# Optimization experiments

Measured on AMD Instinct MI355X. Metric: run time of the kernel, lower is better.

The kernel has to match this reference:

```python
import jax, jax.numpy as jnp
import numpy as np
from jax import lax


def _binarize(t):
    # sign binarization to +1/-1 (zero maps to -1, matching torch.where(t > 0, 1, -1))
    return jnp.where(t > 0, 1.0, -1.0).astype(t.dtype)


def _bconv(x, w, b):
    # binary conv: binarize input and weights, then standard 3x3 'same' conv
    y = lax.conv_general_dilated(
        _binarize(x), _binarize(w),
        window_strides=(1, 1), padding=((1, 1), (1, 1)),
        dimension_numbers=('NCHW', 'OIHW', 'NCHW'))
    return y + b[None, :, None, None]


def _maxpool2(x):
    return lax.reduce_window(x, -jnp.inf, lax.max, (1, 1, 2, 2), (1, 1, 2, 2), 'VALID')


def setup_inputs() -> dict:
    key = jax.random.key(0)
    ks = jax.random.split(key, 13)
    s = 0.1
    return {
        'x': jax.random.normal(ks[0], (4096, 1, 28, 28), jnp.float32),
        'w1': jax.random.normal(ks[1], (32, 1, 3, 3), jnp.float32) * s,
        'b1': jax.random.normal(ks[2], (32,), jnp.float32) * s,
        'w2': jax.random.normal(ks[3], (64, 32, 3, 3), jnp.float32) * s,
        'b2': jax.random.normal(ks[4], (64,), jnp.float32) * s,
        'w3': jax.random.normal(ks[5], (16, 64, 3, 3), jnp.float32) * s,
        'b3': jax.random.normal(ks[6], (16,), jnp.float32) * s,
        'fc1_w': jax.random.normal(ks[7], (256, 16 * 7 * 7), jnp.float32) * s,
        'fc1_b': jax.random.normal(ks[8], (256,), jnp.float32) * s,
        'fc2_w': jax.random.normal(ks[9], (128, 256), jnp.float32) * s,
        'fc2_b': jax.random.normal(ks[10], (128,), jnp.float32) * s,
        'fc3_w': jax.random.normal(ks[11], (10, 128), jnp.float32) * s,
        'fc3_b': jax.random.normal(ks[12], (10,), jnp.float32) * s,
    }


def reference(x, w1, b1, w2, b2, w3, b3, fc1_w, fc1_b, fc2_w, fc2_b, fc3_w, fc3_b):
    h = jax.nn.relu(_maxpool2(_bconv(x, w1, b1)))      # [B,32,14,14]
    h = jax.nn.relu(_maxpool2(_bconv(h, w2, b2)))      # [B,64,7,7]
    h = jax.nn.relu(_bconv(h, w3, b3))                 # [B,16,7,7]
    h = h.reshape(-1, 16 * 7 * 7)
    h = jax.nn.relu(h @ fc1_w.T + fc1_b)
    h = jax.nn.relu(h @ fc2_w.T + fc2_b)
    return h @ fc3_w.T + fc3_b                          # [B,10]
```

## Files before the change

### kernel.cpp

```cpp
#include <hip/hip_runtime.h>
#include <cstdint>

#define OFF_PW    0
#define OFF_W1T   4096
#define OFF_W2T   823296
#define OFF_H3T   954368
#define OFF_H1T   14061568
#define OFF_H2T   18255872

__global__ __launch_bounds__(256) void prep(
    const float* __restrict__ w1, const float* __restrict__ w2,
    const float* __restrict__ w3,
    const float* __restrict__ fc1_w, const float* __restrict__ fc2_w,
    uint32_t* __restrict__ pw, float* __restrict__ w1T, float* __restrict__ w2T) {
    int t = threadIdx.x;
    if (blockIdx.x == 0) {
        if (t < 32) {
            uint32_t b = 0;
            for (int k = 0; k < 9; ++k) b |= (w1[t * 9 + k] > 0.f ? 1u : 0u) << k;
            pw[t] = b;
        }
        for (int idx = t; idx < 576; idx += 256) {
            int oc = idx / 9, tap = idx % 9;
            int kh = tap / 3, kw = tap % 3;
            uint32_t b = 0;
            for (int ic = 0; ic < 32; ++ic)
                b |= (w2[((oc * 32 + ic) * 3 + kh) * 3 + kw] > 0.f ? 1u : 0u) << ic;
            pw[32 + idx] = b;
        }
        for (int idx = t; idx < 144; idx += 256) {
            int oc = idx / 9, tap = idx % 9;
            int kh = tap / 3, kw = tap % 3;
            uint32_t lo = 0, hi = 0;
            for (int ic = 0; ic < 32; ++ic) {
                lo |= (w3[((oc * 64 + ic) * 3 + kh) * 3 + kw] > 0.f ? 1u : 0u) << ic;
                hi |= (w3[((oc * 64 + ic + 32) * 3 + kh) * 3 + kw] > 0.f ? 1u : 0u) << ic;
            }
            pw[608 + idx * 2] = lo;
            pw[608 + idx * 2 + 1] = hi;
        }
    } else {
        int e = (blockIdx.x - 1) * 256 + t;
        if (e < 204800) {
            int k = e >> 8, n = e & 255;
            w1T[e] = (k < 784) ? fc1_w[n * 784 + k] : 0.f;
        } else {
            int e2 = e - 204800;
            int k = e2 >> 7, n = e2 & 127;
            w2T[e2] = fc2_w[n * 256 + k];
        }
    }
}

__global__ __launch_bounds__(256) void conv_stack(
    const float* __restrict__ x,
    const float* __restrict__ b1, const float* __restrict__ b2,
    const float* __restrict__ b3,
    const uint32_t* __restrict__ pw,
    float* __restrict__ h3T) {
    __shared__ uint32_t s_wb1[32];
    __shared__ uint32_t s_W2[576];
    __shared__ uint32_t s_W3[288];
    __shared__ float s_b1[32], s_b2[64], s_b3[16];
    __shared__ uint32_t s_xrow[28];
    __shared__ uint32_t s_H1[256];
    __shared__ uint32_t s_H2[162];

    const int t = threadIdx.x;
    const int img = blockIdx.x;

    s_H1[t] = 0;
    if (t < 162) s_H2[t] = 0;
    if (t < 32) { s_wb1[t] = pw[t]; s_b1[t] = b1[t]; }
    if (t >= 32 && t < 96) s_b2[t - 32] = b2[t - 32];
    if (t >= 96 && t < 112) s_b3[t - 96] = b3[t - 96];
    for (int i = t; i < 576; i += 256) s_W2[i] = pw[32 + i];
    for (int i = t; i < 288; i += 256) s_W3[i] = pw[608 + i];
    if (t >= 192 && t < 220) {
        int r = t - 192;
        const float* xr = x + img * 784 + r * 28;
        uint32_t b = 0;
        for (int j = 0; j < 28; ++j) b |= (xr[j] > 0.f ? 1u : 0u) << j;
        s_xrow[r] = b;
    }
    __syncthreads();

    if (t < 196) {
        int pi = t / 14, pj = t % 14;
        uint32_t sarr[4], marr[4];
        int pcm[4];
#pragma unroll
        for (int p = 0; p < 4; ++p) {
            int i = 2 * pi + (p >> 1), j = 2 * pj + (p & 1);
            uint32_t sb = 0, mb = 0;
            int bit = 0;
#pragma unroll
            for (int di = -1; di <= 1; ++di) {
                int y = i + di;
                bool rv = (unsigned)y < 28u;
                uint32_t row = rv ? s_xrow[rv ? y : 0] : 0u;
#pragma unroll
                for (int dj = -1; dj <= 1; ++dj) {
                    int xx = j + dj;
                    bool v = rv && (unsigned)xx < 28u;
                    if (v) {
                        mb |= 1u << bit;
                        sb |= ((row >> xx) & 1u) << bit;
                    }
                    ++bit;
                }
            }
            sarr[p] = sb; marr[p] = mb; pcm[p] = __popc(mb);
        }
        uint32_t word = 0;
#pragma unroll
        for (int c = 0; c < 32; ++c) {
            uint32_t w = s_wb1[c];
            int best = -1000;
#pragma unroll
            for (int p = 0; p < 4; ++p) {
                int v = pcm[p] - 2 * __popc((sarr[p] ^ w) & marr[p]);
                best = v > best ? v : best;
            }
            word |= ((float)best + s_b1[c] > 0.f ? 1u : 0u) << c;
        }
        s_H1[(pi + 1) * 16 + (pj + 1)] = word;
    }
    __syncthreads();

    for (int task = t; task < 400; task += 256) {
        int q = task / 25, ip = task - q * 25;
        int pi = ip / 5 + 1, pj = ip % 5 + 1;
        uint32_t cell[16];
#pragma unroll
        for (int r = 0; r < 4; ++r)
#pragma unroll
            for (int c = 0; c < 4; ++c)
                cell[r * 4 + c] = s_H1[(2 * pi + r) * 16 + (2 * pj + c)];
        uint32_t nib = 0;
#pragma unroll
        for (int o = 0; o < 4; ++o) {
            int oc = q * 4 + o;
            const uint32_t* wrow = &s_W2[oc * 9];
            int best = -100000;
#pragma unroll
            for (int a = 0; a < 2; ++a)
#pragma unroll
                for (int b = 0; b < 2; ++b) {
                    int S = 0;
#pragma unroll
                    for (int kh = 0; kh < 3; ++kh)
#pragma unroll
                        for (int kw = 0; kw < 3; ++kw)
                            S += __popc(cell[(a + kh) * 4 + (b + kw)] ^ wrow[kh * 3 + kw]);
                    int v = 288 - 2 * S;
                    best = v > best ? v : best;
                }
            nib |= ((float)best + s_b2[oc] > 0.f ? 1u : 0u) << (oc & 31);
        }
        atomicOr((unsigned int*)&s_H2[((pi + 1) * 9 + (pj + 1)) * 2 + (q >> 3)],
                 (unsigned int)nib);
    }
    for (int task = t; task < 384; task += 256) {
        int q = task / 24, bp = task - q * 24;
        int pi, pj;
        if (bp < 7)       { pi = 0; pj = bp; }
        else if (bp < 14) { pi = 6; pj = bp - 7; }
        else if (bp < 19) { pi = bp - 13; pj = 0; }
        else              { pi = bp - 18; pj = 6; }
        uint32_t vr[4], vc[4];
#pragma unroll
        for (int r = 0; r < 4; ++r) {
            vr[r] = ((unsigned)(2 * pi - 1 + r) < 14u) ? 0xFFFFFFFFu : 0u;
            vc[r] = ((unsigned)(2 * pj - 1 + r) < 14u) ? 0xFFFFFFFFu : 0u;
        }
        uint32_t cell[16], V[16];
#pragma unroll
        for (int r = 0; r < 4; ++r)
#pragma unroll
            for (int c = 0; c < 4; ++c) {
                cell[r * 4 + c] = s_H1[(2 * pi + r) * 16 + (2 * pj + c)];
                V[r * 4 + c] = vr[r] & vc[c];
            }
        int nvp[4];
#pragma unroll
        for (int a = 0; a < 2; ++a)
#pragma unroll
            for (int b = 0; b < 2; ++b) {
                int i = 2 * pi + a, j = 2 * pj + b;
                int vy = 3 - (i == 0) - (i == 13);
                int vx = 3 - (j == 0) - (j == 13);
                nvp[a * 2 + b] = 32 * vy * vx;
            }
        uint32_t nib = 0;
#pragma unroll
        for (int o = 0; o < 4; ++o) {
            int oc = q * 4 + o;
            const uint32_t* wrow = &s_W2[oc * 9];
            int best = -100000;
#pragma unroll
            for (int a = 0; a < 2; ++a)
#pragma unroll
                for (int b = 0; b < 2; ++b) {
                    int S = 0;
#pragma unroll
                    for (int kh = 0; kh < 3; ++kh)
#pragma unroll
                        for (int kw = 0; kw < 3; ++kw) {
                            int ci = (a + kh) * 4 + (b + kw);
                            S += __popc((cell[ci] ^ wrow[kh * 3 + kw]) & V[ci]);
                        }
                    int v = nvp[a * 2 + b] - 2 * S;
                    best = v > best ? v : best;
                }
            nib |= ((float)best + s_b2[oc] > 0.f ? 1u : 0u) << (oc & 31);
        }
        atomicOr((unsigned int*)&s_H2[((pi + 1) * 9 + (pj + 1)) * 2 + (q >> 3)],
                 (unsigned int)nib);
    }
    __syncthreads();

    for (int task = t; task < 784; task += 256) {
        int oc = task / 49, pos = task - oc * 49;
        int pi = pos / 7, pj = pos % 7;
        uint32_t vr[3], vc[3];
#pragma unroll
        for (int d = 0; d < 3; ++d) {
            vr[d] = ((unsigned)(pi - 1 + d) < 7u) ? 0xFFFFFFFFu : 0u;
            vc[d] = ((unsigned)(pj - 1 + d) < 7u) ? 0xFFFFFFFFu : 0u;
        }
        int vy = 3 - (pi == 0) - (pi == 6);
        int vx = 3 - (pj == 0) - (pj == 6);
        int Nv = 64 * vy * vx;
        const uint32_t* wr = &s_W3[oc * 18];
        int S = 0;
#pragma unroll
        for (int kh = 0; kh < 3; ++kh)
#pragma unroll
            for (int kw = 0; kw < 3; ++kw) {
                uint32_t V = vr[kh] & vc[kw];
                int idx = ((pi + kh) * 9 + (pj + kw)) * 2;
                S += __popc((s_H2[idx] ^ wr[(kh * 3 + kw) * 2]) & V);
                S += __popc((s_H2[idx + 1] ^ wr[(kh * 3 + kw) * 2 + 1]) & V);
            }
        float h = (float)(Nv - 2 * S) + s_b3[oc];
        h3T[task * 4096 + img] = h > 0.f ? h : 0.f;
    }
}

__global__ __launch_bounds__(256) void fc1_gemm(
    const float* __restrict__ aT,
    const float* __restrict__ bT,
    const float* __restrict__ bias,
    float* __restrict__ oT) {
    const int KC = 80, LD = 68;
    __shared__ float As[KC * LD];
    __shared__ float Bs[KC * LD];
    const int t = threadIdx.x;
    const int tx = t & 15, ty = t >> 4;
    const int img0 = blockIdx.x * 64;
    const int n0 = blockIdx.y * 64;
    float acc[4][4] = {{0.f}};

    for (int kc = 0; kc < 800; kc += KC) {
#pragma unroll
        for (int s = 0; s < 5; ++s) {
            int v = t + s * 256;
            int kk = v >> 4, i4 = (v & 15) * 4;
            *(float4*)&As[kk * LD + i4] =
                *(const float4*)&aT[(kc + kk) * 4096 + img0 + i4];
            *(float4*)&Bs[kk * LD + i4] =
                *(const float4*)&bT[(kc + kk) * 256 + n0 + i4];
        }
        __syncthreads();
#pragma unroll 4
        for (int kk = 0; kk < KC; ++kk) {
            float4 a = *(const float4*)&As[kk * LD + ty * 4];
            float4 b = *(const float4*)&Bs[kk * LD + tx * 4];
            acc[0][0] += a.x * b.x; acc[0][1] += a.x * b.y;
            acc[0][2] += a.x * b.z; acc[0][3] += a.x * b.w;
            acc[1][0] += a.y * b.x; acc[1][1] += a.y * b.y;
            acc[1][2] += a.y * b.z; acc[1][3] += a.y * b.w;
            acc[2][0] += a.z * b.x; acc[2][1] += a.z * b.y;
            acc[2][2] += a.z * b.z; acc[2][3] += a.z * b.w;
            acc[3][0] += a.w * b.x; acc[3][1] += a.w * b.y;
            acc[3][2] += a.w * b.z; acc[3][3] += a.w * b.w;
        }
        __syncthreads();
    }
    float4 bb = *(const float4*)&bias[n0 + tx * 4];
    float bv[4] = {bb.x, bb.y, bb.z, bb.w};
#pragma unroll
    for (int jj = 0; jj < 4; ++jj) {
        float4 ov;
        ov.x = acc[0][jj] + bv[jj]; ov.x = ov.x > 0.f ? ov.x : 0.f;
        ov.y = acc[1][jj] + bv[jj]; ov.y = ov.y > 0.f ? ov.y : 0.f;
        ov.z = acc[2][jj] + bv[jj]; ov.z = ov.z > 0.f ? ov.z : 0.f;
        ov.w = acc[3][jj] + bv[jj]; ov.w = ov.w > 0.f ? ov.w : 0.f;
        *(float4*)&oT[(n0 + tx * 4 + jj) * 4096 + img0 + ty * 4] = ov;
    }
}

__global__ __launch_bounds__(256) void fc2_gemm(
    const float* __restrict__ aT,
    const float* __restrict__ bT,
    const float* __restrict__ bias,
    float* __restrict__ oT) {
    const int KC = 64, LDA = 68, LDB = 36;
    __shared__ float As[KC * LDA];
    __shared__ float Bs[KC * LDB];
    const int t = threadIdx.x;
    const int tx = t & 15, ty = t >> 4;
    const int img0 = blockIdx.x * 64;
    const int n0 = blockIdx.y * 32;
    float acc[4][2] = {{0.f}};

    for (int kc = 0; kc < 256; kc += KC) {
#pragma unroll
        for (int s = 0; s < 4; ++s) {
            int v = t + s * 256;
            int kk = v >> 4, i4 = (v & 15) * 4;
            *(float4*)&As[kk * LDA + i4] =
                *(const float4*)&aT[(kc + kk) * 4096 + img0 + i4];
        }
#pragma unroll
        for (int s = 0; s < 2; ++s) {
            int v = t + s * 256;
            int kk = v >> 3, n4 = (v & 7) * 4;
            *(float4*)&Bs[kk * LDB + n4] =
                *(const float4*)&bT[(kc + kk) * 128 + n0 + n4];
        }
        __syncthreads();
#pragma unroll 4
        for (int kk = 0; kk < KC; ++kk) {
            float4 a = *(const float4*)&As[kk * LDA + ty * 4];
            float2 b = *(const float2*)&Bs[kk * LDB + tx * 2];
            acc[0][0] += a.x * b.x; acc[0][1] += a.x * b.y;
            acc[1][0] += a.y * b.x; acc[1][1] += a.y * b.y;
            acc[2][0] += a.z * b.x; acc[2][1] += a.z * b.y;
            acc[3][0] += a.w * b.x; acc[3][1] += a.w * b.y;
        }
        __syncthreads();
    }
#pragma unroll
    for (int j = 0; j < 2; ++j) {
        int n = n0 + tx * 2 + j;
        float bj = bias[n];
        float4 ov;
        ov.x = acc[0][j] + bj; ov.x = ov.x > 0.f ? ov.x : 0.f;
        ov.y = acc[1][j] + bj; ov.y = ov.y > 0.f ? ov.y : 0.f;
        ov.z = acc[2][j] + bj; ov.z = ov.z > 0.f ? ov.z : 0.f;
        ov.w = acc[3][j] + bj; ov.w = ov.w > 0.f ? ov.w : 0.f;
        *(float4*)&oT[n * 4096 + img0 + ty * 4] = ov;
    }
}

__global__ __launch_bounds__(256) void fc3_gemm(
    const float* __restrict__ aT,
    const float* __restrict__ w,
    const float* __restrict__ bias,
    float* __restrict__ out) {
    int id = blockIdx.x * 256 + threadIdx.x;
    int n = id >> 12, img = id & 4095;
    const float* wr = w + n * 128;
    float a0 = 0.f, a1 = 0.f, a2 = 0.f, a3 = 0.f;
#pragma unroll 8
    for (int k = 0; k < 128; k += 4) {
        a0 += aT[(k + 0) * 4096 + img] * wr[k + 0];
        a1 += aT[(k + 1) * 4096 + img] * wr[k + 1];
        a2 += aT[(k + 2) * 4096 + img] * wr[k + 2];
        a3 += aT[(k + 3) * 4096 + img] * wr[k + 3];
    }
    out[img * 10 + n] = (a0 + a1) + (a2 + a3) + bias[n];
}

extern "C" void kernel_launch(void* const* d_in, const int* in_sizes, int n_in,
                              void* d_out, int out_size, void* d_ws, size_t ws_size,
                              hipStream_t stream) {
    const float* x     = (const float*)d_in[0];
    const float* w1    = (const float*)d_in[1];
    const float* b1    = (const float*)d_in[2];
    const float* w2    = (const float*)d_in[3];
    const float* b2    = (const float*)d_in[4];
    const float* w3    = (const float*)d_in[5];
    const float* b3    = (const float*)d_in[6];
    const float* fc1_w = (const float*)d_in[7];
    const float* fc1_b = (const float*)d_in[8];
    const float* fc2_w = (const float*)d_in[9];
    const float* fc2_b = (const float*)d_in[10];
    const float* fc3_w = (const float*)d_in[11];
    const float* fc3_b = (const float*)d_in[12];
    float* out = (float*)d_out;

    const int B = in_sizes[0] / 784;
    char* ws = (char*)d_ws;
    uint32_t* pw = (uint32_t*)(ws + OFF_PW);
    float* w1T = (float*)(ws + OFF_W1T);
    float* w2T = (float*)(ws + OFF_W2T);
    float* h3T = (float*)(ws + OFF_H3T);
    float* h1T = (float*)(ws + OFF_H1T);
    float* h2T = (float*)(ws + OFF_H2T);

    hipLaunchKernelGGL(prep, dim3(929), dim3(256), 0, stream,
                       w1, w2, w3, fc1_w, fc2_w, pw, w1T, w2T);
    hipLaunchKernelGGL(conv_stack, dim3(B), dim3(256), 0, stream,
                       x, b1, b2, b3, pw, h3T);
    hipLaunchKernelGGL(fc1_gemm, dim3(B / 64, 4), dim3(256), 0, stream,
                       h3T, w1T, fc1_b, h1T);
    hipLaunchKernelGGL(fc2_gemm, dim3(B / 64, 4), dim3(256), 0, stream,
                       h1T, w2T, fc2_b, h2T);
    hipLaunchKernelGGL(fc3_gemm, dim3(B * 10 / 256), dim3(256), 0, stream,
                       h2T, fc3_w, fc3_b, out);
}
```

Baseline: 220.1 us.

## Batch eight images per conv block and retile FC GEMMs

The conv stack now processes eight images per block. conv2 and conv3 are remapped so that each lane owns an output channel and results are packed with wave ballots. Interior positions use a popcount-threshold test with the bias folded into an integer threshold, and border positions get a separate correction path. The prep kernel is flattened into one linear index space and now also zero-pads the h3T tail. fc1 and fc2 are retiled with larger K chunks and smaller N and M tiles, which adds blocks at the cost of more shared memory per block.

```diff
diff --git a/kernel.cpp b/kernel.cpp
--- a/kernel.cpp
+++ b/kernel.cpp
@@ -12,327 +12,330 @@
     const float* __restrict__ w1, const float* __restrict__ w2,
     const float* __restrict__ w3,
     const float* __restrict__ fc1_w, const float* __restrict__ fc2_w,
-    uint32_t* __restrict__ pw, float* __restrict__ w1T, float* __restrict__ w2T) {
-    int t = threadIdx.x;
-    if (blockIdx.x == 0) {
-        if (t < 32) {
-            uint32_t b = 0;
-            for (int k = 0; k < 9; ++k) b |= (w1[t * 9 + k] > 0.f ? 1u : 0u) << k;
-            pw[t] = b;
-        }
-        for (int idx = t; idx < 576; idx += 256) {
-            int oc = idx / 9, tap = idx % 9;
-            int kh = tap / 3, kw = tap % 3;
-            uint32_t b = 0;
-            for (int ic = 0; ic < 32; ++ic)
-                b |= (w2[((oc * 32 + ic) * 3 + kh) * 3 + kw] > 0.f ? 1u : 0u) << ic;
-            pw[32 + idx] = b;
-        }
-        for (int idx = t; idx < 144; idx += 256) {
-            int oc = idx / 9, tap = idx % 9;
-            int kh = tap / 3, kw = tap % 3;
-            uint32_t lo = 0, hi = 0;
-            for (int ic = 0; ic < 32; ++ic) {
-                lo |= (w3[((oc * 64 + ic) * 3 + kh) * 3 + kw] > 0.f ? 1u : 0u) << ic;
-                hi |= (w3[((oc * 64 + ic + 32) * 3 + kh) * 3 + kw] > 0.f ? 1u : 0u) << ic;
-            }
-            pw[608 + idx * 2] = lo;
-            pw[608 + idx * 2 + 1] = hi;
-        }
+    uint32_t* __restrict__ pw, float* __restrict__ w1T,
+    float* __restrict__ w2T, float* __restrict__ h3T) {
+    int idx = blockIdx.x * 256 + threadIdx.x;
+    if (idx < 204800) {
+        int k = idx >> 8, n = idx & 255;
+        w1T[idx] = (k < 784) ? fc1_w[n * 784 + k] : 0.f;
+        return;
+    }
+    idx -= 204800;
+    if (idx < 32768) {
+        int k = idx >> 7, n = idx & 127;
+        w2T[idx] = fc2_w[n * 256 + k];
+        return;
+    }
+    idx -= 32768;
+    if (idx < 65536) {
+        h3T[784 * 4096 + idx] = 0.f;
+        return;
+    }
+    idx -= 65536;
+    if (idx >= 896) return;
+    if (idx < 32) {
+        uint32_t b = 0;
+#pragma unroll
+        for (int k = 0; k < 9; ++k) b |= (w1[idx * 9 + k] > 0.f ? 1u : 0u) << k;
+        pw[idx] = b;
+    } else if (idx < 608) {
+        int e = idx - 32;
+        int oc = e / 9, tap = e - oc * 9;
+        uint32_t b = 0;
+#pragma unroll
+        for (int ic = 0; ic < 32; ++ic)
+            b |= (w2[(oc * 32 + ic) * 9 + tap] > 0.f ? 1u : 0u) << ic;
+        pw[idx] = b;
     } else {
-        int e = (blockIdx.x - 1) * 256 + t;
-        if (e < 204800) {
-            int k = e >> 8, n = e & 255;
-            w1T[e] = (k < 784) ? fc1_w[n * 784 + k] : 0.f;
+        int e = idx - 608;
+        int oc = e / 18, r = e - oc * 18;
+        int tap = r >> 1, half = r & 1;
+        uint32_t b = 0;
+#pragma unroll
+        for (int ic = 0; ic < 32; ++ic)
+            b |= (w3[(oc * 64 + half * 32 + ic) * 9 + tap] > 0.f ? 1u : 0u) << ic;
+        pw[idx] = b;
+    }
+}
+
+__device__ __forceinline__ uint32_t bfe3(uint32_t r, int j) { return (r >> j) & 7u; }
+
+__global__ __launch_bounds__(256, 2) void conv_stack(
+    const float* __restrict__ x, const float* __restrict__ b1,
+    const float* __restrict__ b2, const float* __restrict__ b3,
+    const uint32_t* __restrict__ pw, float* __restrict__ h3T) {
+    __shared__ uint32_t s_xr[8 * 36];
+    __shared__ uint32_t s_H1[8 * 260];
+    __shared__ uint32_t s_H2[8 * 164];
+    __shared__ uint32_t s_w1[32];
+    __shared__ int s_sth1[32], s_ic1[32], s_ic2[64];
+    __shared__ uint32_t s_W2t[576];
+    __shared__ uint32_t s_W3t[288];
+    __shared__ float s_b3[16];
+
+    const int t = threadIdx.x;
+    const int lane = t & 63;
+    const int wid = t >> 6;
+    const int img0 = blockIdx.x * 8;
+
+    for (int i = t; i < 8 * 260; i += 256) s_H1[i] = 0;
+    for (int i = t; i < 8 * 164; i += 256) s_H2[i] = 0;
+    if (t < 224) {
+        int im = t / 28, row = t - im * 28;
+        const float4* xr = (const float4*)(x + (img0 + im) * 784 + row * 28);
+        uint32_t b = 0;
+#pragma unroll
+        for (int q = 0; q < 7; ++q) {
+            float4 v = xr[q];
+            b |= (v.x > 0.f ? 1u : 0u) << (q * 4 + 0);
+            b |= (v.y > 0.f ? 1u : 0u) << (q * 4 + 1);
+            b |= (v.z > 0.f ? 1u : 0u) << (q * 4 + 2);
+            b |= (v.w > 0.f ? 1u : 0u) << (q * 4 + 3);
+        }
+        s_xr[im * 36 + row] = b << 1;
+    }
+    if (t < 32) {
+        s_w1[t] = pw[t];
+        int ic = (int)floorf(-b1[t]) + 1;
+        s_ic1[t] = ic;
+        s_sth1[t] = (9 - ic) >> 1;
+    } else if (t >= 32 && t < 96) {
+        s_ic2[t - 32] = (int)floorf(-b2[t - 32]) + 1;
+    } else if (t >= 96 && t < 112) {
+        s_b3[t - 96] = b3[t - 96];
+    }
+    for (int i = t; i < 576; i += 256)
+        s_W2t[i] = pw[32 + (i & 63) * 9 + (i >> 6)];
+    for (int i = t; i < 288; i += 256)
+        s_W3t[i] = pw[608 + (i & 15) * 18 + (i >> 4)];
+    __syncthreads();
+
+    for (int task = t; task < 1568; task += 256) {
+        int pid = task >> 3, im = task & 7;
+        int pi, pj;
+        if (pid < 144) { pi = 1 + pid / 12; pj = 1 + pid - (pid / 12) * 12; }
+        else {
+            int b = pid - 144;
+            if (b < 14)      { pi = 0;  pj = b; }
+            else if (b < 28) { pi = 13; pj = b - 14; }
+            else if (b < 40) { pi = 1 + (b - 28); pj = 0; }
+            else             { pi = 1 + (b - 40); pj = 13; }
+        }
+        const uint32_t* xr = &s_xr[im * 36];
+        int y0 = 2 * pi - 1;
+        uint32_t r0 = (pi > 0)  ? xr[y0]     : 0u;
+        uint32_t r1 = xr[y0 + 1];
+        uint32_t r2 = xr[y0 + 2];
+        uint32_t r3 = (pi < 13) ? xr[y0 + 3] : 0u;
+        int j0 = 2 * pj, j1 = 2 * pj + 1;
+        uint32_t s00 = bfe3(r0, j0) | (bfe3(r1, j0) << 3) | (bfe3(r2, j0) << 6);
+        uint32_t s01 = bfe3(r0, j1) | (bfe3(r1, j1) << 3) | (bfe3(r2, j1) << 6);
+        uint32_t s10 = bfe3(r1, j0) | (bfe3(r2, j0) << 3) | (bfe3(r3, j0) << 6);
+        uint32_t s11 = bfe3(r1, j1) | (bfe3(r2, j1) << 3) | (bfe3(r3, j1) << 6);
+        uint32_t word = 0;
+        if (pid < 144) {
+#pragma unroll
+            for (int c = 0; c < 32; ++c) {
+                uint32_t w = s_w1[c];
+                int S = min(min(__popc(s00 ^ w), __popc(s01 ^ w)),
+                            min(__popc(s10 ^ w), __popc(s11 ^ w)));
+                word |= (uint32_t)(S <= s_sth1[c]) << c;
+            }
         } else {
-            int e2 = e - 204800;
-            int k = e2 >> 7, n = e2 & 127;
-            w2T[e2] = fc2_w[n * 256 + k];
-        }
-    }
-}
-
-__global__ __launch_bounds__(256) void conv_stack(
-    const float* __restrict__ x,
-    const float* __restrict__ b1, const float* __restrict__ b2,
-    const float* __restrict__ b3,
-    const uint32_t* __restrict__ pw,
-    float* __restrict__ h3T) {
-    __shared__ uint32_t s_wb1[32];
-    __shared__ uint32_t s_W2[576];
-    __shared__ uint32_t s_W3[288];
-    __shared__ float s_b1[32], s_b2[64], s_b3[16];
-    __shared__ uint32_t s_xrow[28];
-    __shared__ uint32_t s_H1[256];
-    __shared__ uint32_t s_H2[162];
-
-    const int t = threadIdx.x;
-    const int img = blockIdx.x;
-
-    s_H1[t] = 0;
-    if (t < 162) s_H2[t] = 0;
-    if (t < 32) { s_wb1[t] = pw[t]; s_b1[t] = b1[t]; }
-    if (t >= 32 && t < 96) s_b2[t - 32] = b2[t - 32];
-    if (t >= 96 && t < 112) s_b3[t - 96] = b3[t - 96];
-    for (int i = t; i < 576; i += 256) s_W2[i] = pw[32 + i];
-    for (int i = t; i < 288; i += 256) s_W3[i] = pw[608 + i];
-    if (t >= 192 && t < 220) {
-        int r = t - 192;
-        const float* xr = x + img * 784 + r * 28;
-        uint32_t b = 0;
-        for (int j = 0; j < 28; ++j) b |= (xr[j] > 0.f ? 1u : 0u) << j;
-        s_xrow[r] = b;
+            uint32_t iT = (pi == 0)  ? 0x7u   : 0u;
+            uint32_t iB = (pi == 13) ? 0x1C0u : 0u;
+            uint32_t iL = (pj == 0)  ? 0x49u  : 0u;
+            uint32_t iR = (pj == 13) ? 0x124u : 0u;
+            uint32_t i00 = iT | iL, i01 = iT | iR, i10 = iB | iL, i11 = iB | iR;
+            int n00 = 9 - __popc(i00), n01 = 9 - __popc(i01);
+            int n10 = 9 - __popc(i10), n11 = 9 - __popc(i11);
+#pragma unroll
+            for (int c = 0; c < 32; ++c) {
+                uint32_t w = s_w1[c];
+                int v0 = n00 - 2 * (__popc(s00 ^ w) - __popc(w & i00));
+                int v1 = n01 - 2 * (__popc(s01 ^ w) - __popc(w & i01));
+                int v2 = n10 - 2 * (__popc(s10 ^ w) - __popc(w & i10));
+                int v3 = n11 - 2 * (__popc(s11 ^ w) - __popc(w & i11));
+                int vm = max(max(v0, v1), max(v2, v3));
+                word |= (uint32_t)(vm >= s_ic1[c]) << c;
+            }
+        }
+        s_H1[im * 260 + (pi + 1) * 16 + (pj + 1)] = word;
     }
     __syncthreads();
 
-    if (t < 196) {
-        int pi = t / 14, pj = t % 14;
-        uint32_t sarr[4], marr[4];
-        int pcm[4];
-#pragma unroll
-        for (int p = 0; p < 4; ++p) {
-            int i = 2 * pi + (p >> 1), j = 2 * pj + (p & 1);
-            uint32_t sb = 0, mb = 0;
-            int bit = 0;
-#pragma unroll
-            for (int di = -1; di <= 1; ++di) {
-                int y = i + di;
-                bool rv = (unsigned)y < 28u;
-                uint32_t row = rv ? s_xrow[rv ? y : 0] : 0u;
-#pragma unroll
-                for (int dj = -1; dj <= 1; ++dj) {
-                    int xx = j + dj;
-                    bool v = rv && (unsigned)xx < 28u;
-                    if (v) {
-                        mb |= 1u << bit;
-                        sb |= ((row >> xx) & 1u) << bit;
-                    }
-                    ++bit;
+    {
+        uint32_t w0 = s_W2t[0 * 64 + lane], w1r = s_W2t[1 * 64 + lane],
+                 w2r = s_W2t[2 * 64 + lane], w3r = s_W2t[3 * 64 + lane],
+                 w4 = s_W2t[4 * 64 + lane], w5 = s_W2t[5 * 64 + lane],
+                 w6 = s_W2t[6 * 64 + lane], w7 = s_W2t[7 * 64 + lane],
+                 w8 = s_W2t[8 * 64 + lane];
+        int ic2 = s_ic2[lane];
+        int sth2 = (288 - ic2) >> 1;
+        int pc0 = __popc(w0), pc1 = __popc(w1r), pc2 = __popc(w2r);
+        int pc3 = __popc(w3r), pc5 = __popc(w5), pc6 = __popc(w6);
+        int pc7 = __popc(w7), pc8 = __popc(w8);
+        int topc = pc0 + pc1 + pc2, botc = pc6 + pc7 + pc8;
+        int lefc = pc0 + pc3 + pc6, rigc = pc2 + pc5 + pc8;
+
+        for (int wt = wid; wt < 392; wt += 4) {
+            int im = wt & 7, pos = wt >> 3;
+            int pi, pj;
+            if (pos < 25) { pi = 1 + pos / 5; pj = 1 + pos - (pos / 5) * 5; }
+            else {
+                int b = pos - 25;
+                if (b < 7)       { pi = 0; pj = b; }
+                else if (b < 14) { pi = 6; pj = b - 7; }
+                else if (b < 19) { pi = b - 13; pj = 0; }
+                else             { pi = b - 18; pj = 6; }
+            }
+            int base = im * 260 + 2 * pi * 16 + 2 * pj;
+            uint2 ra0 = *(const uint2*)&s_H1[base],      ra1 = *(const uint2*)&s_H1[base + 2];
+            uint2 rb0 = *(const uint2*)&s_H1[base + 16], rb1 = *(const uint2*)&s_H1[base + 18];
+            uint2 rc0 = *(const uint2*)&s_H1[base + 32], rc1 = *(const uint2*)&s_H1[base + 34];
+            uint2 rd0 = *(const uint2*)&s_H1[base + 48], rd1 = *(const uint2*)&s_H1[base + 50];
+            uint32_t c00 = ra0.x, c01 = ra0.y, c02 = ra1.x, c03 = ra1.y;
+            uint32_t c10 = rb0.x, c11 = rb0.y, c12 = rb1.x, c13 = rb1.y;
+            uint32_t c20 = rc0.x, c21 = rc0.y, c22 = rc1.x, c23 = rc1.y;
+            uint32_t c30 = rd0.x, c31 = rd0.y, c32 = rd1.x, c33 = rd1.y;
+            int S00 = __popc(c00 ^ w0) + __popc(c01 ^ w1r) + __popc(c02 ^ w2r)
+                    + __popc(c10 ^ w3r) + __popc(c11 ^ w4) + __popc(c12 ^ w5)
+                    + __popc(c20 ^ w6) + __popc(c21 ^ w7) + __popc(c22 ^ w8);
+            int S01 = __popc(c01 ^ w0) + __popc(c02 ^ w1r) + __popc(c03 ^ w2r)
+                    + __popc(c11 ^ w3r) + __popc(c12 ^ w4) + __popc(c13 ^ w5)
+                    + __popc(c21 ^ w6) + __popc(c22 ^ w7) + __popc(c23 ^ w8);
+            int S10 = __popc(c10 ^ w0) + __popc(c11 ^ w1r) + __popc(c12 ^ w2r)
+                    + __popc(c20 ^ w3r) + __popc(c21 ^ w4) + __popc(c22 ^ w5)
+                    + __popc(c30 ^ w6) + __popc(c31 ^ w7) + __popc(c32 ^ w8);
+            int S11 = __popc(c11 ^ w0) + __popc(c12 ^ w1r) + __popc(c13 ^ w2r)
+                    + __popc(c21 ^ w3r) + __popc(c22 ^ w4) + __popc(c23 ^ w5)
+                    + __popc(c31 ^ w6) + __popc(c32 ^ w7) + __popc(c33 ^ w8);
+            int pred;
+            if (pos < 25) {
+                int Sm = min(min(S00, S01), min(S10, S11));
+                pred = (Sm <= sth2);
+            } else {
+                int vmax;
+                {
+                    int rI = (pi == 0), cI = (pj == 0);
+                    int corr = (rI ? topc : 0) + (cI ? lefc : 0) - ((rI & cI) ? pc0 : 0);
+                    int nv = 32 * (9 - 3 * rI - 3 * cI + (rI & cI));
+                    vmax = nv - 2 * (S00 - corr);
                 }
-            }
-            sarr[p] = sb; marr[p] = mb; pcm[p] = __popc(mb);
-        }
-        uint32_t word = 0;
-#pragma unroll
-        for (int c = 0; c < 32; ++c) {
-            uint32_t w = s_wb1[c];
-            int best = -1000;
-#pragma unroll
-            for (int p = 0; p < 4; ++p) {
-                int v = pcm[p] - 2 * __popc((sarr[p] ^ w) & marr[p]);
-                best = v > best ? v : best;
-            }
-            word |= ((float)best + s_b1[c] > 0.f ? 1u : 0u) << c;
-        }
-        s_H1[(pi + 1) * 16 + (pj + 1)] = word;
+                {
+                    int rI = (pi == 0), cI = (pj == 6);
+                    int corr = (rI ? topc : 0) + (cI ? rigc : 0) - ((rI & cI) ? pc2 : 0);
+                    int nv = 32 * (9 - 3 * rI - 3 * cI + (rI & cI));
+                    vmax = max(vmax, nv - 2 * (S01 - corr));
+                }
+                {
+                    int rI = (pi == 6), cI = (pj == 0);
+                    int corr = (rI ? botc : 0) + (cI ? lefc : 0) - ((rI & cI) ? pc6 : 0);
+                    int nv = 32 * (9 - 3 * rI - 3 * cI + (rI & cI));
+                    vmax = max(vmax, nv - 2 * (S10 - corr));
+                }
+                {
+                    int rI = (pi == 6), cI = (pj == 6);
+                    int corr = (rI ? botc : 0) + (cI ? rigc : 0) - ((rI & cI) ? pc8 : 0);
+                    int nv = 32 * (9 - 3 * rI - 3 * cI + (rI & cI));
+                    vmax = max(vmax, nv - 2 * (S11 - corr));
+                }
+                pred = (vmax >= ic2);
+            }
+            unsigned long long m = __ballot(pred);
+            if (lane == 0) {
+                *(uint2*)&s_H2[im * 164 + ((pi + 1) * 9 + (pj + 1)) * 2] =
+                    make_uint2((uint32_t)m, (uint32_t)(m >> 32));
+            }
+        }
     }
     __syncthreads();
 
-    for (int task = t; task < 400; task += 256) {
-        int q = task / 25, ip = task - q * 25;
-        int pi = ip / 5 + 1, pj = ip % 5 + 1;
-        uint32_t cell[16];
-#pragma unroll
-        for (int r = 0; r < 4; ++r)
-#pragma unroll
-            for (int c = 0; c < 4; ++c)
-                cell[r * 4 + c] = s_H1[(2 * pi + r) * 16 + (2 * pj + c)];
-        uint32_t nib = 0;
-#pragma unroll
-        for (int o = 0; o < 4; ++o) {
-            int oc = q * 4 + o;
-            const uint32_t* wrow = &s_W2[oc * 9];
-            int best = -100000;
-#pragma unroll
-            for (int a = 0; a < 2; ++a)
-#pragma unroll
-                for (int b = 0; b < 2; ++b) {
-                    int S = 0;
-#pragma unroll
-                    for (int kh = 0; kh < 3; ++kh)
-#pragma unroll
-                        for (int kw = 0; kw < 3; ++kw)
-                            S += __popc(cell[(a + kh) * 4 + (b + kw)] ^ wrow[kh * 3 + kw]);
-                    int v = 288 - 2 * S;
-                    best = v > best ? v : best;
+    {
+        int oc = lane & 15, iq = lane >> 4;
+        uint32_t w[18];
+#pragma unroll
+        for (int k = 0; k < 18; ++k) w[k] = s_W3t[k * 16 + oc];
+        float bias3 = s_b3[oc];
+        int pc[9];
+#pragma unroll
+        for (int k = 0; k < 9; ++k) pc[k] = __popc(w[2 * k]) + __popc(w[2 * k + 1]);
+        int topc = pc[0] + pc[1] + pc[2], botc = pc[6] + pc[7] + pc[8];
+        int lefc = pc[0] + pc[3] + pc[6], rigc = pc[2] + pc[5] + pc[8];
+
+        for (int wt = wid; wt < 98; wt += 4) {
+            int iq2 = wt & 1, pos = wt >> 1;
+            int im = iq2 * 4 + iq;
+            int pi, pj;
+            if (pos < 25) { pi = 1 + pos / 5; pj = 1 + pos - (pos / 5) * 5; }
+            else {
+                int b = pos - 25;
+                if (b < 7)       { pi = 0; pj = b; }
+                else if (b < 14) { pi = 6; pj = b - 7; }
+                else if (b < 19) { pi = b - 13; pj = 0; }
+                else             { pi = b - 18; pj = 6; }
+            }
+            const uint32_t* hp = &s_H2[im * 164];
+            int S = 0;
+#pragma unroll
+            for (int kh = 0; kh < 3; ++kh)
+#pragma unroll
+                for (int kw = 0; kw < 3; ++kw) {
+                    uint2 cc = *(const uint2*)&hp[((pi + kh) * 9 + (pj + kw)) * 2];
+                    int k = kh * 3 + kw;
+                    S += __popc(cc.x ^ w[2 * k]) + __popc(cc.y ^ w[2 * k + 1]);
                 }
-            nib |= ((float)best + s_b2[oc] > 0.f ? 1u : 0u) << (oc & 31);
-        }
-        atomicOr((unsigned int*)&s_H2[((pi + 1) * 9 + (pj + 1)) * 2 + (q >> 3)],
-                 (unsigned int)nib);
-    }
-    for (int task = t; task < 384; task += 256) {
-        int q = task / 24, bp = task - q * 24;
-        int pi, pj;
-        if (bp < 7)       { pi = 0; pj = bp; }
-        else if (bp < 14) { pi = 6; pj = bp - 7; }
-        else if (bp < 19) { pi = bp - 13; pj = 0; }
-        else              { pi = bp - 18; pj = 6; }
-        uint32_t vr[4], vc[4];
-#pragma unroll
-        for (int r = 0; r < 4; ++r) {
-            vr[r] = ((unsigned)(2 * pi - 1 + r) < 14u) ? 0xFFFFFFFFu : 0u;
-            vc[r] = ((unsigned)(2 * pj - 1 + r) < 14u) ? 0xFFFFFFFFu : 0u;
-        }
-        uint32_t cell[16], V[16];
-#pragma unroll
-        for (int r = 0; r < 4; ++r)
-#pragma unroll
-            for (int c = 0; c < 4; ++c) {
-                cell[r * 4 + c] = s_H1[(2 * pi + r) * 16 + (2 * pj + c)];
-                V[r * 4 + c] = vr[r] & vc[c];
-            }
-        int nvp[4];
-#pragma unroll
-        for (int a = 0; a < 2; ++a)
-#pragma unroll
-            for (int b = 0; b < 2; ++b) {
-                int i = 2 * pi + a, j = 2 * pj + b;
-                int vy = 3 - (i == 0) - (i == 13);
-                int vx = 3 - (j == 0) - (j == 13);
-                nvp[a * 2 + b] = 32 * vy * vx;
-            }
-        uint32_t nib = 0;
-#pragma unroll
-        for (int o = 0; o < 4; ++o) {
-            int oc = q * 4 + o;
-            const uint32_t* wrow = &s_W2[oc * 9];
-            int best = -100000;
-#pragma unroll
-            for (int a = 0; a < 2; ++a)
-#pragma unroll
-                for (int b = 0; b < 2; ++b) {
-                    int S = 0;
-#pragma unroll
-                    for (int kh = 0; kh < 3; ++kh)
-#pragma unroll
-                        for (int kw = 0; kw < 3; ++kw) {
-                            int ci = (a + kh) * 4 + (b + kw);
-                            S += __popc((cell[ci] ^ wrow[kh * 3 + kw]) & V[ci]);
-                        }
-                    int v = nvp[a * 2 + b] - 2 * S;
-                    best = v > best ? v : best;
-                }
-            nib |= ((float)best + s_b2[oc] > 0.f ? 1u : 0u) << (oc & 31);
-        }
-        atomicOr((unsigned int*)&s_H2[((pi + 1) * 9 + (pj + 1)) * 2 + (q >> 3)],
-                 (unsigned int)nib);
-    }
-    __syncthreads();
-
-    for (int task = t; task < 784; task += 256) {
-        int oc = task / 49, pos = task - oc * 49;
-        int pi = pos / 7, pj = pos % 7;
-        uint32_t vr[3], vc[3];
-#pragma unroll
-        for (int d = 0; d < 3; ++d) {
-            vr[d] = ((unsigned)(pi - 1 + d) < 7u) ? 0xFFFFFFFFu : 0u;
-            vc[d] = ((unsigned)(pj - 1 + d) < 7u) ? 0xFFFFFFFFu : 0u;
-        }
-        int vy = 3 - (pi == 0) - (pi == 6);
-        int vx = 3 - (pj == 0) - (pj == 6);
-        int Nv = 64 * vy * vx;
-        const uint32_t* wr = &s_W3[oc * 18];
-        int S = 0;
-#pragma unroll
-        for (int kh = 0; kh < 3; ++kh)
-#pragma unroll
-            for (int kw = 0; kw < 3; ++kw) {
-                uint32_t V = vr[kh] & vc[kw];
-                int idx = ((pi + kh) * 9 + (pj + kw)) * 2;
-                S += __popc((s_H2[idx] ^ wr[(kh * 3 + kw) * 2]) & V);
-                S += __popc((s_H2[idx + 1] ^ wr[(kh * 3 + kw) * 2 + 1]) & V);
-            }
-        float h = (float)(Nv - 2 * S) + s_b3[oc];
-        h3T[task * 4096 + img] = h > 0.f ? h : 0.f;
-    }
-}
-
-__global__ __launch_bounds__(256) void fc1_gemm(
-    const float* __restrict__ aT,
-    const float* __restrict__ bT,
-    const float* __restrict__ bias,
-    float* __restrict__ oT) {
-    const int KC = 80, LD = 68;
-    __shared__ float As[KC * LD];
-    __shared__ float Bs[KC * LD];
-    const int t = threadIdx.x;
-    const int tx = t & 15, ty = t >> 4;
-    const int img0 = blockIdx.x * 64;
-    const int n0 = blockIdx.y * 64;
-    float acc[4][4] = {{0.f}};
-
-    for (int kc = 0; kc < 800; kc += KC) {
-#pragma unroll
-        for (int s = 0; s < 5; ++s) {
-            int v = t + s * 256;
-            int kk = v >> 4, i4 = (v & 15) * 4;
-            *(float4*)&As[kk * LD + i4] =
-                *(const float4*)&aT[(kc + kk) * 4096 + img0 + i4];
-            *(float4*)&Bs[kk * LD + i4] =
-                *(const float4*)&bT[(kc + kk) * 256 + n0 + i4];
-        }
-        __syncthreads();
-#pragma unroll 4
-        for (int kk = 0; kk < KC; ++kk) {
-            float4 a = *(const float4*)&As[kk * LD + ty * 4];
-            float4 b = *(const float4*)&Bs[kk * LD + tx * 4];
-            acc[0][0] += a.x * b.x; acc[0][1] += a.x * b.y;
-            acc[0][2] += a.x * b.z; acc[0][3] += a.x * b.w;
-            acc[1][0] += a.y * b.x; acc[1][1] += a.y * b.y;
-            acc[1][2] += a.y * b.z; acc[1][3] += a.y * b.w;
-            acc[2][0] += a.z * b.x; acc[2][1] += a.z * b.y;
-            acc[2][2] += a.z * b.z; acc[2][3] += a.z * b.w;
-            acc[3][0] += a.w * b.x; acc[3][1] += a.w * b.y;
-            acc[3][2] += a.w * b.z; acc[3][3] += a.w * b.w;
-        }
-        __syncthreads();
-    }
-    float4 bb = *(const float4*)&bias[n0 + tx * 4];
-    float bv[4] = {bb.x, bb.y, bb.z, bb.w};
-#pragma unroll
-    for (int jj = 0; jj < 4; ++jj) {
-        float4 ov;
-        ov.x = acc[0][jj] + bv[jj]; ov.x = ov.x > 0.f ? ov.x : 0.f;
-        ov.y = acc[1][jj] + bv[jj]; ov.y = ov.y > 0.f ? ov.y : 0.f;
-        ov.z = acc[2][jj] + bv[jj]; ov.z = ov.z > 0.f ? ov.z : 0.f;
-        ov.w = acc[3][jj] + bv[jj]; ov.w = ov.w > 0.f ? ov.w : 0.f;
-        *(float4*)&oT[(n0 + tx * 4 + jj) * 4096 + img0 + ty * 4] = ov;
-    }
-}
-
-__global__ __launch_bounds__(256) void fc2_gemm(
-    const float* __restrict__ aT,
-    const float* __restrict__ bT,
-    const float* __restrict__ bias,
-    float* __restrict__ oT) {
-    const int KC = 64, LDA = 68, LDB = 36;
-    __shared__ float As[KC * LDA];
-    __shared__ float Bs[KC * LDB];
+            int v;
+            if (pos < 25) {
+                v = 576 - 2 * S;
+            } else {
+                int rT = (pi == 0), rB = (pi == 6), cL = (pj == 0), cR = (pj == 6);
+                int rA = rT | rB, cA = cL | cR;
+                int corr = (rT ? topc : 0) + (rB ? botc : 0) +
+                           (cL ? lefc : 0) + (cR ? rigc : 0);
+                if (rT & cL) corr -= pc[0];
+                if (rT & cR) corr -= pc[2];
+                if (rB & cL) corr -= pc[6];
+                if (rB & cR) corr -= pc[8];
+                int nInv = 3 * rA + 3 * cA - (rA & cA);
+                v = 64 * (9 - nInv) - 2 * (S - corr);
+            }
+            float h = fmaxf((float)v + bias3, 0.f);
+            h3T[(oc * 49 + pi * 7 + pj) * 4096 + img0 + im] = h;
+        }
+    }
+}
+
+__global__ __launch_bounds__(256, 2) void fc1_gemm(
+    const float* __restrict__ aT, const float* __restrict__ bT,
+    const float* __restrict__ bias, float* __restrict__ oT) {
+    const int LDA = 68, LDB = 36;
+    __shared__ float As[160 * LDA];
+    __shared__ float Bs[160 * LDB];
     const int t = threadIdx.x;
     const int tx = t & 15, ty = t >> 4;
     const int img0 = blockIdx.x * 64;
     const int n0 = blockIdx.y * 32;
     float acc[4][2] = {{0.f}};
 
-    for (int kc = 0; kc < 256; kc += KC) {
-#pragma unroll
-        for (int s = 0; s < 4; ++s) {
+    for (int kc = 0; kc < 800; kc += 160) {
+#pragma unroll
+        for (int s = 0; s < 10; ++s) {
             int v = t + s * 256;
-            int kk = v >> 4, i4 = (v & 15) * 4;
-            *(float4*)&As[kk * LDA + i4] =
-                *(const float4*)&aT[(kc + kk) * 4096 + img0 + i4];
-        }
-#pragma unroll
-        for (int s = 0; s < 2; ++s) {
+            int kk = v >> 4, q = (v & 15) * 4;
+            *(float4*)&As[kk * LDA + q] =
+                *(const float4*)&aT[(kc + kk) * 4096 + img0 + q];
+        }
+#pragma unroll
+        for (int s = 0; s < 5; ++s) {
             int v = t + s * 256;
-            int kk = v >> 3, n4 = (v & 7) * 4;
-            *(float4*)&Bs[kk * LDB + n4] =
-                *(const float4*)&bT[(kc + kk) * 128 + n0 + n4];
+            int kk = v >> 3, q = (v & 7) * 4;
+            *(float4*)&Bs[kk * LDB + q] =
+                *(const float4*)&bT[(kc + kk) * 256 + n0 + q];
         }
         __syncthreads();
-#pragma unroll 4
-        for (int kk = 0; kk < KC; ++kk) {
+#pragma unroll 8
+        for (int kk = 0; kk < 160; ++kk) {
             float4 a = *(const float4*)&As[kk * LDA + ty * 4];
             float2 b = *(const float2*)&Bs[kk * LDB + tx * 2];
             acc[0][0] += a.x * b.x; acc[0][1] += a.x * b.y;
@@ -347,19 +350,55 @@
         int n = n0 + tx * 2 + j;
         float bj = bias[n];
         float4 ov;
-        ov.x = acc[0][j] + bj; ov.x = ov.x > 0.f ? ov.x : 0.f;
-        ov.y = acc[1][j] + bj; ov.y = ov.y > 0.f ? ov.y : 0.f;
-        ov.z = acc[2][j] + bj; ov.z = ov.z > 0.f ? ov.z : 0.f;
-        ov.w = acc[3][j] + bj; ov.w = ov.w > 0.f ? ov.w : 0.f;
+        ov.x = fmaxf(acc[0][j] + bj, 0.f);
+        ov.y = fmaxf(acc[1][j] + bj, 0.f);
+        ov.z = fmaxf(acc[2][j] + bj, 0.f);
+        ov.w = fmaxf(acc[3][j] + bj, 0.f);
         *(float4*)&oT[n * 4096 + img0 + ty * 4] = ov;
     }
 }
 
+__global__ __launch_bounds__(256, 2) void fc2_gemm(
+    const float* __restrict__ aT, const float* __restrict__ bT,
+    const float* __restrict__ bias, float* __restrict__ oT) {
+    const int LD = 36;
+    __shared__ float As[256 * LD];
+    __shared__ float Bs[256 * LD];
+    const int t = threadIdx.x;
+    const int tx = t & 15, ty = t >> 4;
+    const int img0 = blockIdx.x * 32;
+    const int n0 = blockIdx.y * 32;
+    float acc[2][2] = {{0.f}};
+
+#pragma unroll
+    for (int s = 0; s < 8; ++s) {
+        int v = t + s * 256;
+        int kk = v >> 3, q = (v & 7) * 4;
+        *(float4*)&As[kk * LD + q] = *(const float4*)&aT[kk * 4096 + img0 + q];
+        *(float4*)&Bs[kk * LD + q] = *(const float4*)&bT[kk * 128 + n0 + q];
+    }
+    __syncthreads();
+#pragma unroll 8
+    for (int kk = 0; kk < 256; ++kk) {
+        float2 a = *(const float2*)&As[kk * LD + ty * 2];
+        float2 b = *(const float2*)&Bs[kk * LD + tx * 2];
+        acc[0][0] += a.x * b.x; acc[0][1] += a.x * b.y;
+        acc[1][0] += a.y * b.x; acc[1][1] += a.y * b.y;
+    }
+#pragma unroll
+    for (int j = 0; j < 2; ++j) {
+        int n = n0 + tx * 2 + j;
+        float bj = bias[n];
+        float2 ov;
+        ov.x = fmaxf(acc[0][j] + bj, 0.f);
+        ov.y = fmaxf(acc[1][j] + bj, 0.f);
+        *(float2*)&oT[n * 4096 + img0 + ty * 2] = ov;
+    }
+}
+
 __global__ __launch_bounds__(256) void fc3_gemm(
-    const float* __restrict__ aT,
-    const float* __restrict__ w,
-    const float* __restrict__ bias,
-    float* __restrict__ out) {
+    const float* __restrict__ aT, const float* __restrict__ w,
+    const float* __restrict__ bias, float* __restrict__ out) {
     int id = blockIdx.x * 256 + threadIdx.x;
     int n = id >> 12, img = id & 4095;
     const float* wr = w + n * 128;
@@ -401,13 +440,13 @@
     float* h1T = (float*)(ws + OFF_H1T);
     float* h2T = (float*)(ws + OFF_H2T);
 
-    hipLaunchKernelGGL(prep, dim3(929), dim3(256), 0, stream,
-                       w1, w2, w3, fc1_w, fc2_w, pw, w1T, w2T);
-    hipLaunchKernelGGL(conv_stack, dim3(B), dim3(256), 0, stream,
+    hipLaunchKernelGGL(prep, dim3(1188), dim3(256), 0, stream,
+                       w1, w2, w3, fc1_w, fc2_w, pw, w1T, w2T, h3T);
+    hipLaunchKernelGGL(conv_stack, dim3(B / 8), dim3(256), 0, stream,
                        x, b1, b2, b3, pw, h3T);
-    hipLaunchKernelGGL(fc1_gemm, dim3(B / 64, 4), dim3(256), 0, stream,
+    hipLaunchKernelGGL(fc1_gemm, dim3(B / 64, 8), dim3(256), 0, stream,
                        h3T, w1T, fc1_b, h1T);
-    hipLaunchKernelGGL(fc2_gemm, dim3(B / 64, 4), dim3(256), 0, stream,
+    hipLaunchKernelGGL(fc2_gemm, dim3(B / 32, 4), dim3(256), 0, stream,
                        h1T, w2T, fc2_b, h2T);
     hipLaunchKernelGGL(fc3_gemm, dim3(B * 10 / 256), dim3(256), 0, stream,
                        h2T, fc3_w, fc3_b, out);
```

Result: slower. 224.9 us (+2.2%).
